# Performance work log

Hardware: AMD Instinct MI355X
Metric: run time of the kernel (lower is better)

Reference implementation:

```python
import jax, jax.numpy as jnp
import numpy as np

EPS = 1e-6
NUM_HEADS = 16


def rms_norm(x, w):
    # x: [..., D], normalize over last dim, learnable scale w [D]
    var = jnp.mean(jnp.square(x), axis=-1, keepdims=True)
    return x * jax.lax.rsqrt(var + EPS) * w


def setup_inputs() -> dict:
    key = jax.random.key(0)
    ks = jax.random.split(key, 6)
    B, N, C = 8, 1024, 1024
    return {
        "x": jax.random.normal(ks[0], (B, N, C), dtype=jnp.float32),
        "w_qkv": jax.random.normal(ks[1], (3 * C, C), dtype=jnp.float32) * (1.0 / np.sqrt(C)),
        "b_qkv": jax.random.normal(ks[2], (3 * C,), dtype=jnp.float32) * 0.02,
        "qn_w": jnp.ones((C // NUM_HEADS,), dtype=jnp.float32),
        "kn_w": jnp.ones((C // NUM_HEADS,), dtype=jnp.float32),
        "w_proj": jax.random.normal(ks[3], (C, C), dtype=jnp.float32) * (1.0 / np.sqrt(C)),
        "b_proj": jax.random.normal(ks[4], (C,), dtype=jnp.float32) * 0.02,
    }


def reference(x, w_qkv, b_qkv, qn_w, kn_w, w_proj, b_proj):
    B, N, C = x.shape
    H = NUM_HEADS
    D = C // H
    # QKV projection: [B,N,3C] -> [3,B,H,N,D]
    qkv = x @ w_qkv.T + b_qkv
    qkv = qkv.reshape(B, N, 3, H, D).transpose(2, 0, 3, 1, 4)
    q, k, v = qkv[0], qkv[1], qkv[2]
    q = rms_norm(q, qn_w)
    k = rms_norm(k, kn_w)
    # scaled dot-product attention (no mask, no dropout in eval)
    scale = 1.0 / np.sqrt(D).astype(np.float32)
    attn = jnp.einsum('bhld,bhsd->bhls', q, k) * scale  # [B,H,N,N]
    attn = jax.nn.softmax(attn, axis=-1)
    out = jnp.einsum('bhls,bhsd->bhld', attn, v)  # [B,H,N,D]
    out = out.transpose(0, 2, 1, 3).reshape(B, N, C)
    return out @ w_proj.T + b_proj
```

## Files before the change

### kernel.cpp

```cpp
#include <hip/hip_runtime.h>
#include <hip/hip_bf16.h>
#include <stdint.h>

#define M_ROWS 8192
#define C_DIM  1024
#define QKV_N  3072

typedef _Float16 f16;
typedef __attribute__((ext_vector_type(8))) _Float16 f16x8;
typedef __attribute__((ext_vector_type(8))) short short8_t;
typedef __attribute__((ext_vector_type(4))) float float4_t;
typedef unsigned short u16;
typedef unsigned int u32;

__device__ __forceinline__ u16 f16_bits(float x) {
  union { f16 h; u16 u; } c; c.h = (f16)x; return c.u;
}
__device__ __forceinline__ u16 f32_to_bf16(float f) {
  u32 u = __float_as_uint(f);
  u32 r = (u + 0x7fffu + ((u >> 16) & 1u)) >> 16;
  return (u16)r;
}
__device__ __forceinline__ float bf16_to_f32(u16 h) {
  return __uint_as_float((u32)h << 16);
}
__device__ __forceinline__ void gld_lds16(const void* g, void* l) {
  __builtin_amdgcn_global_load_lds(
      (const __attribute__((address_space(1))) u32*)g,
      (__attribute__((address_space(3))) u32*)l, 16, 0, 0);
}
__device__ __forceinline__ int elem_off(int row, int e0) {
  return row * 64 + (e0 ^ ((row & 7) << 3));
}

__global__ __launch_bounds__(256) void split_bf16(
    const float* __restrict__ in, u16* __restrict__ hi, u16* __restrict__ lo) {
  int i = blockIdx.x * 256 + threadIdx.x;
  float4 v = ((const float4*)in)[i];
  float x[4] = {v.x, v.y, v.z, v.w};
  union { u16 u[4]; uint2 v2; } H, L;
#pragma unroll
  for (int j = 0; j < 4; ++j) {
    u16 h = f32_to_bf16(x[j]);
    H.u[j] = h;
    L.u[j] = f32_to_bf16(x[j] - bf16_to_f32(h));
  }
  ((uint2*)hi)[i] = H.v2;
  ((uint2*)lo)[i] = L.v2;
}

template <int MODE>
__global__ __launch_bounds__(256) void gemm_split(
    const u16* __restrict__ Ah, const u16* __restrict__ Al,
    const u16* __restrict__ Bh, const u16* __restrict__ Bl,
    const float* __restrict__ bias, void* __restrict__ O0,
    void* __restrict__ O1, void* __restrict__ O2,
    const float* __restrict__ qn_w, const float* __restrict__ kn_w,
    int M, int N, int K) {
  __shared__ u16 sAh[128 * 32], sAl[128 * 32], sBh[128 * 32], sBl[128 * 32];
  const int t = threadIdx.x;
  const int wv = t >> 6;
  const int lane = t & 63;
  const int n0 = blockIdx.x * 128;
  const int m0 = blockIdx.y * 128;
  const int wm = wv >> 1, wn = wv & 1;
  const int fr = lane & 15;
  const int g = lane >> 4;
  const int kfr = g * 8;

  float4_t acc[4][4];
  const float4_t zero = {0.f, 0.f, 0.f, 0.f};
#pragma unroll
  for (int i = 0; i < 4; ++i)
#pragma unroll
    for (int j = 0; j < 4; ++j) acc[i][j] = zero;

  for (int k0 = 0; k0 < K; k0 += 32) {
#pragma unroll
    for (int u = 0; u < 2; ++u) {
      int idx = u * 256 + t;
      int row = idx >> 2;
      int ke = (idx & 3) * 8;
      int ldsoff = (u * 256 + wv * 64) * 8;
      const size_t ga = (size_t)(m0 + row) * K + k0 + ke;
      const size_t gb = (size_t)(n0 + row) * K + k0 + ke;
      gld_lds16(Ah + ga, sAh + ldsoff);
      gld_lds16(Al + ga, sAl + ldsoff);
      gld_lds16(Bh + gb, sBh + ldsoff);
      gld_lds16(Bl + gb, sBl + ldsoff);
    }
    __syncthreads();

    short8_t ah[4], al[4], bh[4], bl[4];
#pragma unroll
    for (int i = 0; i < 4; ++i) {
      ah[i] = *(const short8_t*)&sAh[(wm * 64 + i * 16 + fr) * 32 + kfr];
      al[i] = *(const short8_t*)&sAl[(wm * 64 + i * 16 + fr) * 32 + kfr];
      bh[i] = *(const short8_t*)&sBh[(wn * 64 + i * 16 + fr) * 32 + kfr];
      bl[i] = *(const short8_t*)&sBl[(wn * 64 + i * 16 + fr) * 32 + kfr];
    }
#pragma unroll
    for (int i = 0; i < 4; ++i)
#pragma unroll
      for (int j = 0; j < 4; ++j) {
        acc[i][j] = __builtin_amdgcn_mfma_f32_16x16x32_bf16(ah[i], bh[j], acc[i][j], 0, 0, 0);
        acc[i][j] = __builtin_amdgcn_mfma_f32_16x16x32_bf16(ah[i], bl[j], acc[i][j], 0, 0, 0);
        acc[i][j] = __builtin_amdgcn_mfma_f32_16x16x32_bf16(al[i], bh[j], acc[i][j], 0, 0, 0);
      }
    __syncthreads();
  }

  const int r0 = g * 4;
  const int nw = n0 + wn * 64;
  float bz[4];
#pragma unroll
  for (int j = 0; j < 4; ++j) bz[j] = bias[nw + j * 16 + fr];

  if (MODE == 0) {
    const int sec = nw >> 10;
    const int h = (nw >> 6) & 15;
    u16* O = (sec == 0) ? (u16*)O0 : ((sec == 1) ? (u16*)O1 : (u16*)O2);
    float wn_[4];
    if (sec < 2) {
      const float* wvec = (sec == 0) ? qn_w : kn_w;
#pragma unroll
      for (int j = 0; j < 4; ++j) wn_[j] = wvec[j * 16 + fr];
    }
#pragma unroll
    for (int i = 0; i < 4; ++i) {
      float val[4][4];
#pragma unroll
      for (int j = 0; j < 4; ++j)
#pragma unroll
        for (int r = 0; r < 4; ++r) val[j][r] = acc[i][j][r] + bz[j];
      if (sec < 2) {
#pragma unroll
        for (int r = 0; r < 4; ++r) {
          float ss = 0.f;
#pragma unroll
          for (int j = 0; j < 4; ++j) ss += val[j][r] * val[j][r];
#pragma unroll
          for (int mask = 8; mask >= 1; mask >>= 1) ss += __shfl_xor(ss, mask);
          float sc = rsqrtf(ss * (1.0f / 64.0f) + 1e-6f);
#pragma unroll
          for (int j = 0; j < 4; ++j) val[j][r] *= sc * wn_[j];
        }
      }
#pragma unroll
      for (int j = 0; j < 4; ++j) {
        int col = h * 64 + j * 16 + fr;
#pragma unroll
        for (int r = 0; r < 4; ++r) {
          int m = m0 + wm * 64 + i * 16 + r0 + r;
          O[(size_t)m * 1024 + col] = f16_bits(val[j][r]);
        }
      }
    }
  } else {
    float* O = (float*)O0;
#pragma unroll
    for (int j = 0; j < 4; ++j) {
      int n = nw + j * 16 + fr;
#pragma unroll
      for (int i = 0; i < 4; ++i) {
        int mb = m0 + wm * 64 + i * 16 + r0;
#pragma unroll
        for (int r = 0; r < 4; ++r)
          O[(size_t)(mb + r) * 1024 + n] = acc[i][j][r] + bz[j];
      }
    }
  }
}

__global__ __launch_bounds__(256) void vtrans16(const u16* __restrict__ v,
                                                u16* __restrict__ vt) {
  __shared__ __align__(16) u16 T[64][80];
  const int t = threadIdx.x;
  const int nb = blockIdx.x;
  const int bh = blockIdx.y;
  const int b = bh >> 4, h = bh & 15;
  const int n0 = nb * 64;
#pragma unroll
  for (int u = 0; u < 2; ++u) {
    int idx = u * 256 + t;
    int row = idx >> 3;
    int c8 = (idx & 7) * 8;
    uint4 val = *(const uint4*)&v[((size_t)(b * 1024 + n0 + row)) * 1024 + h * 64 + c8];
    *(uint4*)&T[row][c8] = val;
  }
  __syncthreads();
#pragma unroll
  for (int u = 0; u < 2; ++u) {
    int idx = u * 256 + t;
    int d = idx >> 3;
    int n8 = (idx & 7) * 8;
    union { u16 q[8]; uint4 v4; } P;
#pragma unroll
    for (int i = 0; i < 8; ++i) P.q[i] = T[n8 + i][d];
    *(uint4*)&vt[((size_t)bh * 64 + d) * 1024 + n0 + n8] = P.v4;
  }
}

__device__ __forceinline__ void stage_tile64(const u16* __restrict__ src,
                                             u16* __restrict__ lds, int t,
                                             int rowbase, size_t stride,
                                             int colbase) {
#pragma unroll
  for (int u = 0; u < 2; ++u) {
    int idx = u * 256 + t;
    int row = idx >> 3;
    int cs = (idx & 7) ^ (row & 7);
    gld_lds16(src + (size_t)(rowbase + row) * stride + colbase + cs * 8,
              lds + (size_t)(u * 256 + (t >> 6) * 64) * 8);
  }
}

__global__ __launch_bounds__(256) void flash_f16(
    const u16* __restrict__ q, const u16* __restrict__ k,
    const u16* __restrict__ vt, u16* __restrict__ ao_hi,
    u16* __restrict__ ao_lo) {
  __shared__ __align__(16) u16 sK[2][4096];
  __shared__ __align__(16) u16 sV[2][4096];
  __shared__ __align__(16) u16 sP[4][16][88];
  const int t = threadIdx.x;
  const int wv = t >> 6, lane = t & 63;
  const int fr = lane & 15;
  const int g = lane >> 4;
  int flat = blockIdx.x;
  int nf = (flat & 7) * 256 + (flat >> 3);
  const int qb = nf & 15, bh = nf >> 4;
  const int q0 = qb * 64;
  const int b = bh >> 4, h = bh & 15;

  const u16* qrow = q + ((size_t)(b * 1024 + q0 + wv * 16 + fr)) * 1024 + h * 64;
  const u16* krow = k + ((size_t)b * 1024) * 1024 + h * 64;
  const u16* vbase = vt + (size_t)bh * 64 * 1024;

  f16x8 aQ[2];
#pragma unroll
  for (int c = 0; c < 2; ++c)
    aQ[c] = *(const f16x8*)&qrow[c * 32 + g * 8];

  float m_run = -1e30f, l_run = 0.f;
  float4_t o[4];
  const float4_t zero = {0.f, 0.f, 0.f, 0.f};
#pragma unroll
  for (int dt = 0; dt < 4; ++dt) o[dt] = zero;
  const float scale = 0.125f;

  stage_tile64(krow, &sK[0][0], t, 0, 1024, 0);
  stage_tile64(vbase, &sV[0][0], t, 0, 1024, 0);
  __syncthreads();

  int cur = 0;
  for (int it = 0; it < 16; ++it) {
    const int k0 = it * 64;
    if (it < 15) {
      stage_tile64(krow, &sK[cur ^ 1][0], t, k0 + 64, 1024, 0);
      stage_tile64(vbase, &sV[cur ^ 1][0], t, 0, 1024, k0 + 64);
    }
    const u16* sKc = &sK[cur][0];
    const u16* sVc = &sV[cur][0];

    float4_t sac[4];
#pragma unroll
    for (int j = 0; j < 4; ++j) sac[j] = zero;
#pragma unroll
    for (int j = 0; j < 4; ++j) {
      f16x8 kb0 = *(const f16x8*)&sKc[elem_off(j * 16 + fr, g * 8)];
      f16x8 kb1 = *(const f16x8*)&sKc[elem_off(j * 16 + fr, 32 + g * 8)];
      __builtin_amdgcn_s_setprio(1);
      sac[j] = __builtin_amdgcn_mfma_f32_16x16x32_f16(kb0, aQ[0], sac[j], 0, 0, 0);
      sac[j] = __builtin_amdgcn_mfma_f32_16x16x32_f16(kb1, aQ[1], sac[j], 0, 0, 0);
      __builtin_amdgcn_s_setprio(0);
    }

    float sv[4][4];
    float pmax = -1e30f;
#pragma unroll
    for (int j = 0; j < 4; ++j)
#pragma unroll
      for (int r = 0; r < 4; ++r) {
        sv[j][r] = sac[j][r] * scale;
        pmax = fmaxf(pmax, sv[j][r]);
      }
    pmax = fmaxf(pmax, __shfl_xor(pmax, 16));
    pmax = fmaxf(pmax, __shfl_xor(pmax, 32));
    float m_new = fmaxf(m_run, pmax);
    float corr = __expf(m_run - m_new);
    float rs = 0.f;
#pragma unroll
    for (int j = 0; j < 4; ++j) {
      union { u16 u[4]; uint2 v2; } P;
#pragma unroll
      for (int r = 0; r < 4; ++r) {
        float p = __expf(sv[j][r] - m_new);
        rs += p;
        P.u[r] = f16_bits(p);
      }
      *(uint2*)&sP[wv][fr][j * 16 + g * 4] = P.v2;
    }
    rs += __shfl_xor(rs, 16);
    rs += __shfl_xor(rs, 32);
    l_run = fmaf(l_run, corr, rs);
    m_run = m_new;

#pragma unroll
    for (int r = 0; r < 4; ++r) {
      float cr = __shfl(corr, (lane & 48) + ((lane >> 4) << 2) + r);
#pragma unroll
      for (int dt = 0; dt < 4; ++dt) o[dt][r] *= cr;
    }

    f16x8 pa[2];
#pragma unroll
    for (int c = 0; c < 2; ++c)
      pa[c] = *(const f16x8*)&sP[wv][fr][c * 32 + g * 8];
#pragma unroll
    for (int dt = 0; dt < 4; ++dt) {
      f16x8 vb0 = *(const f16x8*)&sVc[elem_off(dt * 16 + fr, g * 8)];
      f16x8 vb1 = *(const f16x8*)&sVc[elem_off(dt * 16 + fr, 32 + g * 8)];
      __builtin_amdgcn_s_setprio(1);
      o[dt] = __builtin_amdgcn_mfma_f32_16x16x32_f16(pa[0], vb0, o[dt], 0, 0, 0);
      o[dt] = __builtin_amdgcn_mfma_f32_16x16x32_f16(pa[1], vb1, o[dt], 0, 0, 0);
      __builtin_amdgcn_s_setprio(0);
    }

    __syncthreads();
    cur ^= 1;
  }

#pragma unroll
  for (int r = 0; r < 4; ++r) {
    float lq = __shfl(l_run, (lane & 48) + ((lane >> 4) << 2) + r);
    float inv = 1.0f / lq;
    int qg = q0 + wv * 16 + g * 4 + r;
#pragma unroll
    for (int dt = 0; dt < 4; ++dt) {
      float v = o[dt][r] * inv;
      u16 hb = f32_to_bf16(v);
      size_t off = ((size_t)(b * 1024 + qg)) * 1024 + h * 64 + dt * 16 + fr;
      ao_hi[off] = hb;
      ao_lo[off] = f32_to_bf16(v - bf16_to_f32(hb));
    }
  }
}

extern "C" void kernel_launch(void* const* d_in, const int* in_sizes, int n_in,
                              void* d_out, int out_size, void* d_ws, size_t ws_size,
                              hipStream_t stream) {
  const float* x      = (const float*)d_in[0];
  const float* w_qkv  = (const float*)d_in[1];
  const float* b_qkv  = (const float*)d_in[2];
  const float* qn_w   = (const float*)d_in[3];
  const float* kn_w   = (const float*)d_in[4];
  const float* w_proj = (const float*)d_in[5];
  const float* b_proj = (const float*)d_in[6];
  float* out = (float*)d_out;

  u16* x_hi  = (u16*)d_ws;
  u16* x_lo  = x_hi + 8388608;
  u16* wq_hi = x_lo + 8388608;
  u16* wq_lo = wq_hi + 3145728;
  u16* wp_hi = wq_lo + 3145728;
  u16* wp_lo = wp_hi + 1048576;
  u16* qb    = wp_lo + 1048576;
  u16* kb    = qb + 8388608;
  u16* vb    = kb + 8388608;
  u16* vtb   = vb + 8388608;
  u16* ao_hi = vtb + 8388608;
  u16* ao_lo = ao_hi + 8388608;

  split_bf16<<<8192, 256, 0, stream>>>(x, x_hi, x_lo);
  split_bf16<<<3072, 256, 0, stream>>>(w_qkv, wq_hi, wq_lo);
  split_bf16<<<1024, 256, 0, stream>>>(w_proj, wp_hi, wp_lo);

  gemm_split<0><<<dim3(QKV_N / 128, M_ROWS / 128), 256, 0, stream>>>(
      x_hi, x_lo, wq_hi, wq_lo, b_qkv, qb, kb, vb, qn_w, kn_w,
      M_ROWS, QKV_N, C_DIM);

  vtrans16<<<dim3(16, 128), 256, 0, stream>>>(vb, vtb);

  flash_f16<<<2048, 256, 0, stream>>>(qb, kb, vtb, ao_hi, ao_lo);

  gemm_split<1><<<dim3(C_DIM / 128, M_ROWS / 128), 256, 0, stream>>>(
      ao_hi, ao_lo, wp_hi, wp_lo, b_proj, out, nullptr, nullptr,
      nullptr, nullptr, M_ROWS, C_DIM, C_DIM);
}
```

Before: 403.7 us.

## Double flash query tile to 128 rows and pass P through shuffles instead of LDS

The flash attention kernel now runs 512 threads (8 waves) per block covering 128 query rows, so each staged K/V tile is reused by twice as many waves and each thread issues one async load per tile. The softmax probability matrix is packed to f16 in registers and rearranged into the MFMA A-operand layout with cross-lane shuffles, which removes the per-wave sP LDS buffer along with its store/load round trip. The cost is more shuffle instructions and a larger block, which lowers the number of blocks in the grid and can change occupancy.

```diff
diff --git a/kernel.cpp b/kernel.cpp
--- a/kernel.cpp
+++ b/kernel.cpp
@@ -201,35 +201,30 @@
   }
 }
 
-__device__ __forceinline__ void stage_tile64(const u16* __restrict__ src,
-                                             u16* __restrict__ lds, int t,
-                                             int rowbase, size_t stride,
-                                             int colbase) {
-#pragma unroll
-  for (int u = 0; u < 2; ++u) {
-    int idx = u * 256 + t;
-    int row = idx >> 3;
-    int cs = (idx & 7) ^ (row & 7);
-    gld_lds16(src + (size_t)(rowbase + row) * stride + colbase + cs * 8,
-              lds + (size_t)(u * 256 + (t >> 6) * 64) * 8);
-  }
-}
-
-__global__ __launch_bounds__(256) void flash_f16(
+__device__ __forceinline__ void stage_tile64_512(const u16* __restrict__ src,
+                                                 u16* __restrict__ lds, int t,
+                                                 int rowbase, size_t stride,
+                                                 int colbase) {
+  int row = t >> 3;
+  int cs = (t & 7) ^ (row & 7);
+  gld_lds16(src + (size_t)(rowbase + row) * stride + colbase + cs * 8,
+            lds + (size_t)t * 8);
+}
+
+__global__ __launch_bounds__(512) void flash_f16(
     const u16* __restrict__ q, const u16* __restrict__ k,
     const u16* __restrict__ vt, u16* __restrict__ ao_hi,
     u16* __restrict__ ao_lo) {
   __shared__ __align__(16) u16 sK[2][4096];
   __shared__ __align__(16) u16 sV[2][4096];
-  __shared__ __align__(16) u16 sP[4][16][88];
   const int t = threadIdx.x;
   const int wv = t >> 6, lane = t & 63;
   const int fr = lane & 15;
   const int g = lane >> 4;
   int flat = blockIdx.x;
-  int nf = (flat & 7) * 256 + (flat >> 3);
-  const int qb = nf & 15, bh = nf >> 4;
-  const int q0 = qb * 64;
+  int nf = (flat & 7) * 128 + (flat >> 3);
+  const int qb = nf & 7, bh = nf >> 3;
+  const int q0 = qb * 128;
   const int b = bh >> 4, h = bh & 15;
 
   const u16* qrow = q + ((size_t)(b * 1024 + q0 + wv * 16 + fr)) * 1024 + h * 64;
@@ -248,16 +243,16 @@
   for (int dt = 0; dt < 4; ++dt) o[dt] = zero;
   const float scale = 0.125f;
 
-  stage_tile64(krow, &sK[0][0], t, 0, 1024, 0);
-  stage_tile64(vbase, &sV[0][0], t, 0, 1024, 0);
+  stage_tile64_512(krow, &sK[0][0], t, 0, 1024, 0);
+  stage_tile64_512(vbase, &sV[0][0], t, 0, 1024, 0);
   __syncthreads();
 
   int cur = 0;
   for (int it = 0; it < 16; ++it) {
     const int k0 = it * 64;
     if (it < 15) {
-      stage_tile64(krow, &sK[cur ^ 1][0], t, k0 + 64, 1024, 0);
-      stage_tile64(vbase, &sV[cur ^ 1][0], t, 0, 1024, k0 + 64);
+      stage_tile64_512(krow, &sK[cur ^ 1][0], t, k0 + 64, 1024, 0);
+      stage_tile64_512(vbase, &sV[cur ^ 1][0], t, 0, 1024, k0 + 64);
     }
     const u16* sKc = &sK[cur][0];
     const u16* sVc = &sV[cur][0];
@@ -289,16 +284,16 @@
     float m_new = fmaxf(m_run, pmax);
     float corr = __expf(m_run - m_new);
     float rs = 0.f;
+    u32 pk[4][2];
 #pragma unroll
     for (int j = 0; j < 4; ++j) {
-      union { u16 u[4]; uint2 v2; } P;
-#pragma unroll
-      for (int r = 0; r < 4; ++r) {
-        float p = __expf(sv[j][r] - m_new);
-        rs += p;
-        P.u[r] = f16_bits(p);
-      }
-      *(uint2*)&sP[wv][fr][j * 16 + g * 4] = P.v2;
+      float p0 = __expf(sv[j][0] - m_new);
+      float p1 = __expf(sv[j][1] - m_new);
+      float p2 = __expf(sv[j][2] - m_new);
+      float p3 = __expf(sv[j][3] - m_new);
+      rs += (p0 + p1) + (p2 + p3);
+      pk[j][0] = (u32)f16_bits(p0) | ((u32)f16_bits(p1) << 16);
+      pk[j][1] = (u32)f16_bits(p2) | ((u32)f16_bits(p3) << 16);
     }
     rs += __shfl_xor(rs, 16);
     rs += __shfl_xor(rs, 32);
@@ -312,10 +307,29 @@
       for (int dt = 0; dt < 4; ++dt) o[dt][r] *= cr;
     }
 
+    const int s0 = fr + ((g & 1) << 5);
+    const int s1 = s0 + 16;
+    const bool hi = ((g >> 1) & 1) != 0;
     f16x8 pa[2];
 #pragma unroll
-    for (int c = 0; c < 2; ++c)
-      pa[c] = *(const f16x8*)&sP[wv][fr][c * 32 + g * 8];
+    for (int c = 0; c < 2; ++c) {
+      const int jA = 2 * c, jB = 2 * c + 1;
+      u32 a0 = (u32)__shfl((int)pk[jA][0], s0);
+      u32 a1 = (u32)__shfl((int)pk[jA][1], s0);
+      u32 b0 = (u32)__shfl((int)pk[jB][0], s0);
+      u32 b1 = (u32)__shfl((int)pk[jB][1], s0);
+      u32 a2 = (u32)__shfl((int)pk[jA][0], s1);
+      u32 a3 = (u32)__shfl((int)pk[jA][1], s1);
+      u32 b2 = (u32)__shfl((int)pk[jB][0], s1);
+      u32 b3 = (u32)__shfl((int)pk[jB][1], s1);
+      union { u32 w[4]; f16x8 v; } U;
+      U.w[0] = hi ? b0 : a0;
+      U.w[1] = hi ? b1 : a1;
+      U.w[2] = hi ? b2 : a2;
+      U.w[3] = hi ? b3 : a3;
+      pa[c] = U.v;
+    }
+
 #pragma unroll
     for (int dt = 0; dt < 4; ++dt) {
       f16x8 vb0 = *(const f16x8*)&sVc[elem_off(dt * 16 + fr, g * 8)];
@@ -381,7 +395,7 @@
 
   vtrans16<<<dim3(16, 128), 256, 0, stream>>>(vb, vtb);
 
-  flash_f16<<<2048, 256, 0, stream>>>(qb, kb, vtb, ao_hi, ao_lo);
+  flash_f16<<<1024, 512, 0, stream>>>(qb, kb, vtb, ao_hi, ao_lo);
 
   gemm_split<1><<<dim3(C_DIM / 128, M_ROWS / 128), 256, 0, stream>>>(
       ao_hi, ao_lo, wp_hi, wp_lo, b_proj, out, nullptr, nullptr,
```

After: 401.6 us. About the same (-0.5%).
